# Kernel optimization log

Hardware: AMD Instinct MI355X
Metric: run time of the kernel (lower is better)

The kernel has to match this reference:

```python
import jax, jax.numpy as jnp
import numpy as np

H = 128
N_CAN = 100000
N_FLAG = 50000
E = 600000
L = 500000


def _sage_conv(x_src, x_dst, edge_index, Wl, bl, Wr):
    # PyG SAGEConv (mean aggr): lin_l(mean_{j in N(i)} x_j) + lin_r(x_i)
    src, dst = edge_index[0], edge_index[1]
    msg = x_src[src]                                        # [E, H] gather
    n_dst = x_dst.shape[0]
    agg = jax.ops.segment_sum(msg, dst, num_segments=n_dst)  # [N_dst, H]
    cnt = jax.ops.segment_sum(jnp.ones((msg.shape[0],), msg.dtype), dst,
                              num_segments=n_dst)
    mean = agg / jnp.maximum(cnt, 1.0)[:, None]
    return mean @ Wl.T + bl + x_dst @ Wr.T


def setup_inputs() -> dict:
    key = jax.random.key(0)
    ks = jax.random.split(key, 16)
    s = 1.0 / np.sqrt(H)
    inp = {
        'can_node_id': jnp.arange(N_CAN, dtype=jnp.int64) if jax.config.jax_enable_x64 else jnp.arange(N_CAN, dtype=jnp.int32),
        'flag_node_id': jnp.arange(N_FLAG, dtype=jnp.int32),
        'edge_index_cf': jnp.stack([
            jax.random.randint(ks[0], (E,), 0, N_CAN),
            jax.random.randint(ks[1], (E,), 0, N_FLAG)]),
        'edge_index_fc': jnp.stack([
            jax.random.randint(ks[2], (E,), 0, N_FLAG),
            jax.random.randint(ks[3], (E,), 0, N_CAN)]),
        'edge_label_index': jnp.stack([
            jax.random.randint(ks[4], (L,), 0, N_CAN),
            jax.random.randint(ks[5], (L,), 0, N_FLAG)]),
        'can_emb': jax.random.normal(ks[6], (N_CAN, H), jnp.float32),
        'flag_emb': jax.random.normal(ks[7], (N_FLAG, H), jnp.float32),
        # SAGEConv for edge type CAN->flag (updates flag nodes)
        'Wl_cf': jax.random.normal(ks[8], (H, H), jnp.float32) * s,
        'bl_cf': jnp.zeros((H,), jnp.float32),
        'Wr_cf': jax.random.normal(ks[9], (H, H), jnp.float32) * s,
        # SAGEConv for edge type flag->CAN (updates CAN nodes)
        'Wl_fc': jax.random.normal(ks[10], (H, H), jnp.float32) * s,
        'bl_fc': jnp.zeros((H,), jnp.float32),
        'Wr_fc': jax.random.normal(ks[11], (H, H), jnp.float32) * s,
        # classifier MLP
        'W1': jax.random.normal(ks[12], (H, 2 * H), jnp.float32) * (1.0 / np.sqrt(2 * H)),
        'b1': jnp.zeros((H,), jnp.float32),
        'W2': jax.random.normal(ks[13], (1, H), jnp.float32) * s,
        'b2': jnp.zeros((1,), jnp.float32),
    }
    return inp


def reference(can_node_id, flag_node_id, edge_index_cf, edge_index_fc,
              edge_label_index, can_emb, flag_emb,
              Wl_cf, bl_cf, Wr_cf, Wl_fc, bl_fc, Wr_fc,
              W1, b1, W2, b2):
    # embedding lookups
    x_can = can_emb[can_node_id]    # [N_CAN, H]
    x_flag = flag_emb[flag_node_id]  # [N_FLAG, H]
    # to_hetero single SAGE layer + relu (dropout is identity in eval)
    upd_flag = jax.nn.relu(_sage_conv(x_can, x_flag, edge_index_cf, Wl_cf, bl_cf, Wr_cf))
    upd_can = jax.nn.relu(_sage_conv(x_flag, x_can, edge_index_fc, Wl_fc, bl_fc, Wr_fc))
    # link prediction classifier
    src = upd_can[edge_label_index[0]]   # [L, H]
    dst = upd_flag[edge_label_index[1]]  # [L, H]
    h = jax.nn.relu(jnp.concatenate([src, dst], axis=-1) @ W1.T + b1)
    out = h @ W2.T + b2
    return out.reshape(-1)
```

## Files before the change

### kernel.cpp

```cpp
#include <hip/hip_runtime.h>
#include <hip/hip_bf16.h>

#define H 128
#define BSH 8
#define MAXB 1024
#define PCH 1024
#define PIT (PCH / 256)

typedef __attribute__((ext_vector_type(8))) short short8;
typedef __attribute__((ext_vector_type(4))) short short4v;
typedef __attribute__((ext_vector_type(4))) float floatx4;
typedef unsigned short ushort_t;
typedef unsigned int uint_t;

__device__ __forceinline__ short f2bf(float f) {
    __hip_bfloat16 h = __float2bfloat16(f);
    return *reinterpret_cast<short*>(&h);
}
__device__ __forceinline__ float bflo(uint_t u) { return __uint_as_float(u << 16); }
__device__ __forceinline__ float bfhi(uint_t u) { return __uint_as_float(u & 0xFFFF0000u); }
__device__ __forceinline__ uint_t pack_bf2(float x, float y) {
    return (uint_t)(ushort_t)f2bf(x) | ((uint_t)(ushort_t)f2bf(y) << 16);
}
__device__ __forceinline__ void acc8(float* acc, uint4 r) {
    acc[0] += bflo(r.x); acc[1] += bfhi(r.x);
    acc[2] += bflo(r.y); acc[3] += bfhi(r.y);
    acc[4] += bflo(r.z); acc[5] += bfhi(r.z);
    acc[6] += bflo(r.w); acc[7] += bfhi(r.w);
}

__global__ __launch_bounds__(256)
void bucket_hist_cvt_kernel(const int* __restrict__ ei1, const int* __restrict__ ei2,
                            int E, int NF, int B, int* __restrict__ bcnt, int nbh,
                            const float* __restrict__ a, int n4a,
                            const float* __restrict__ b, int n4b,
                            ushort_t* __restrict__ da, ushort_t* __restrict__ db,
                            const float* __restrict__ Wl_cf, const float* __restrict__ Wr_cf,
                            const float* __restrict__ Wl_fc, const float* __restrict__ Wr_fc,
                            const float* __restrict__ W1, ushort_t* __restrict__ wb) {
    __shared__ int h[MAXB];
    int tid = threadIdx.x;
    if ((int)blockIdx.x < nbh) {
        for (int i = tid; i < B; i += 256) h[i] = 0;
        __syncthreads();
        int base = blockIdx.x * PCH;
        #pragma unroll
        for (int it = 0; it < PIT; ++it) {
            int t = base + it * 256 + tid;
            if (t < 2 * E) {
                int g = (t < E) ? ei1[E + t] : (ei2[E + t - E] + NF);
                atomicAdd(&h[g >> BSH], 1);
            }
        }
        __syncthreads();
        for (int i = tid; i < B; i += 256)
            if (h[i]) atomicAdd(&bcnt[i], h[i]);
        return;
    }
    int i = ((int)blockIdx.x - nbh) * 256 + tid;
    const float* src; ushort_t* dst; int k;
    if (i < n4a) { src = a; dst = da; k = i; }
    else if (i < n4a + n4b) { src = b; dst = db; k = i - n4a; }
    else {
        int idx = (i - n4a - n4b) * 4;
        if (idx >= 98304) return;
        int off;
        if      (idx < 16384) { src = Wl_cf; off = idx; }
        else if (idx < 32768) { src = Wr_cf; off = idx - 16384; }
        else if (idx < 49152) { src = Wl_fc; off = idx - 32768; }
        else if (idx < 65536) { src = Wr_fc; off = idx - 49152; }
        else                  { src = W1;    off = idx - 65536; }
        float4 v = *(const float4*)(src + off);
        short4v s;
        s[0] = f2bf(v.x); s[1] = f2bf(v.y); s[2] = f2bf(v.z); s[3] = f2bf(v.w);
        *(short4v*)(wb + idx) = s;
        return;
    }
    float4 v = ((const float4*)src)[k];
    short4v s;
    s[0] = f2bf(v.x); s[1] = f2bf(v.y); s[2] = f2bf(v.z); s[3] = f2bf(v.w);
    ((short4v*)dst)[k] = s;
}

__global__ __launch_bounds__(256)
void partition_kernel(const int* __restrict__ ei1, const int* __restrict__ ei2,
                      int E, int NF, int B, const int* __restrict__ bcnt,
                      int* __restrict__ bfront, uint_t* __restrict__ part) {
    __shared__ int h[MAXB];
    __shared__ int basex[MAXB];
    __shared__ int sdata[256];
    int tid = threadIdx.x;
    {
        int base4 = tid * 4;
        int v[4]; int s = 0;
        #pragma unroll
        for (int i = 0; i < 4; ++i) { int idx = base4 + i; v[i] = (idx < B) ? bcnt[idx] : 0; s += v[i]; }
        sdata[tid] = s;
        __syncthreads();
        for (int off = 1; off < 256; off <<= 1) {
            int t = (tid >= off) ? sdata[tid - off] : 0;
            __syncthreads();
            sdata[tid] += t;
            __syncthreads();
        }
        int excl = tid ? sdata[tid - 1] : 0;
        #pragma unroll
        for (int i = 0; i < 4; ++i) {
            int idx = base4 + i;
            if (idx < B) basex[idx] = excl;
            excl += v[i];
        }
    }
    for (int i = tid; i < B; i += 256) h[i] = 0;
    __syncthreads();
    int base = blockIdx.x * PCH;
    #pragma unroll
    for (int it = 0; it < PIT; ++it) {
        int t = base + it * 256 + tid;
        if (t < 2 * E) {
            int g = (t < E) ? ei1[E + t] : (ei2[E + t - E] + NF);
            atomicAdd(&h[g >> BSH], 1);
        }
    }
    __syncthreads();
    for (int i = tid; i < B; i += 256) {
        int c = h[i];
        if (c) basex[i] += atomicAdd(&bfront[i], c);
    }
    __syncthreads();
    for (int i = tid; i < B; i += 256) h[i] = 0;
    __syncthreads();
    #pragma unroll
    for (int it = 0; it < PIT; ++it) {
        int t = base + it * 256 + tid;
        if (t < 2 * E) {
            int g, s;
            if (t < E) { g = ei1[E + t]; s = ei1[t]; }
            else       { int e = t - E; g = ei2[E + e] + NF; s = ei2[e]; }
            int bk = g >> BSH;
            int r = atomicAdd(&h[bk], 1);
            part[basex[bk] + r] = ((uint_t)(g & 255) << 24) | (uint_t)s;
        }
    }
}

__global__ __launch_bounds__(256)
void fine_bin_kernel(const int* __restrict__ bcnt, int B, int nTot, int E2,
                     const uint_t* __restrict__ part,
                     int* __restrict__ offs, int* __restrict__ bins) {
    __shared__ int cnt[256];
    __shared__ int sdata[256];
    __shared__ int excl[256];
    int b = blockIdx.x;
    int tid = threadIdx.x;
    {
        int partial = 0;
        for (int i = tid; i < b; i += 256) partial += bcnt[i];
        sdata[tid] = partial;
        __syncthreads();
        for (int off = 128; off > 0; off >>= 1) {
            if (tid < off) sdata[tid] += sdata[tid + off];
            __syncthreads();
        }
    }
    int seg0 = sdata[0];
    int seg1 = seg0 + bcnt[b];
    int gbase = b << BSH;
    __syncthreads();
    cnt[tid] = 0;
    __syncthreads();
    for (int k = seg0 + tid; k < seg1; k += 256)
        atomicAdd(&cnt[part[k] >> 24], 1);
    __syncthreads();
    sdata[tid] = cnt[tid];
    __syncthreads();
    for (int off = 1; off < 256; off <<= 1) {
        int t = (tid >= off) ? sdata[tid - off] : 0;
        __syncthreads();
        sdata[tid] += t;
        __syncthreads();
    }
    excl[tid] = tid ? sdata[tid - 1] : 0;
    int g = gbase + tid;
    if (g < nTot) offs[g] = seg0 + excl[tid];
    if (b == 0 && tid == 0) offs[nTot] = E2;
    cnt[tid] = 0;
    __syncthreads();
    for (int k = seg0 + tid; k < seg1; k += 256) {
        uint_t e = part[k];
        int l = (int)(e >> 24);
        int r = atomicAdd(&cnt[l], 1);
        bins[seg0 + excl[l] + r] = (int)(e & 0x00FFFFFFu);
    }
}

__global__ __launch_bounds__(256)
void gather_mean16_kernel(const int* __restrict__ offs, int nTotal, int split,
                          const int* __restrict__ bins,
                          const ushort_t* __restrict__ embA, ushort_t* __restrict__ aggA,
                          const ushort_t* __restrict__ embB, ushort_t* __restrict__ aggB) {
    int g = blockIdx.x * 16 + (threadIdx.x >> 4);
    if (g >= nTotal) return;
    int l15 = threadIdx.x & 15;
    int start = offs[g];
    int end = offs[g + 1];
    int deg = end - start;
    const ushort_t* emb; ushort_t* agg; int row;
    if (g < split) { emb = embA; agg = aggA; row = g; }
    else           { emb = embB; agg = aggB; row = g - split; }

    float acc[8];
    #pragma unroll
    for (int t = 0; t < 8; ++t) acc[t] = 0.f;

    const ushort_t* ep = emb + l15 * 8;
    int nPre = deg < 16 ? deg : 16;
    int pre = (l15 < nPre) ? bins[start + l15] : 0;

    int k = 0;
    for (; k + 3 < nPre; k += 4) {
        int s0 = __shfl(pre, k,     16);
        int s1 = __shfl(pre, k + 1, 16);
        int s2 = __shfl(pre, k + 2, 16);
        int s3 = __shfl(pre, k + 3, 16);
        uint4 r0 = *(const uint4*)(ep + (size_t)s0 * H);
        uint4 r1 = *(const uint4*)(ep + (size_t)s1 * H);
        uint4 r2 = *(const uint4*)(ep + (size_t)s2 * H);
        uint4 r3 = *(const uint4*)(ep + (size_t)s3 * H);
        acc8(acc, r0); acc8(acc, r1); acc8(acc, r2); acc8(acc, r3);
    }
    for (; k < nPre; ++k) {
        int s = __shfl(pre, k, 16);
        uint4 r = *(const uint4*)(ep + (size_t)s * H);
        acc8(acc, r);
    }
    for (int kk = start + 16; kk < end; ++kk) {
        int s = bins[kk];
        uint4 r = *(const uint4*)(ep + (size_t)s * H);
        acc8(acc, r);
    }

    float inv = 1.0f / fmaxf((float)deg, 1.0f);
    uint4 o;
    o.x = pack_bf2(acc[0] * inv, acc[1] * inv);
    o.y = pack_bf2(acc[2] * inv, acc[3] * inv);
    o.z = pack_bf2(acc[4] * inv, acc[5] * inv);
    o.w = pack_bf2(acc[6] * inv, acc[7] * inv);
    *(uint4*)(agg + (size_t)row * H + l15 * 8) = o;
}

__global__ __launch_bounds__(256)
void sage3_kernel(int nbF, int NF, int NC,
                  ushort_t* __restrict__ aggf, const ushort_t* __restrict__ embf,
                  ushort_t* __restrict__ aggc, const ushort_t* __restrict__ embc,
                  const ushort_t* __restrict__ wlf, const ushort_t* __restrict__ wrf,
                  const float* __restrict__ blf,
                  const ushort_t* __restrict__ wlc, const ushort_t* __restrict__ wrc,
                  const float* __restrict__ blc,
                  const ushort_t* __restrict__ W1) {
    __shared__ short A[64][136];
    bool isF = (int)blockIdx.x < nbF;
    int nrows = isF ? NF : NC;
    int rbase = (isF ? blockIdx.x : blockIdx.x - nbF) * 64;
    ushort_t* io = isF ? aggf : aggc;
    const ushort_t* emb = isF ? embf : embc;
    const ushort_t* Wl = isF ? wlf : wlc;
    const ushort_t* Wr = isF ? wrf : wrc;
    const float* bl = isF ? blf : blc;
    int koff = isF ? 128 : 0;

    int tid = threadIdx.x;
    int lane = tid & 63;
    int wv = tid >> 6;
    int l15 = lane & 15;
    int quad = lane >> 4;
    int nb0 = 32 * wv + l15;

    floatx4 acc[4][2];
    #pragma unroll
    for (int i = 0; i < 4; ++i)
        #pragma unroll
        for (int j = 0; j < 2; ++j)
            acc[i][j] = (floatx4){0.f, 0.f, 0.f, 0.f};

    float blv0 = bl[nb0];
    float blv1 = bl[nb0 + 16];

    for (int idx = tid; idx < 64 * 16; idx += 256) {
        int r = idx >> 4, c = idx & 15;
        int row = rbase + r;
        uint4 v = (uint4){0u, 0u, 0u, 0u};
        if (row < nrows) v = *(const uint4*)(io + (size_t)row * H + c * 8);
        *(uint4*)&A[r][c * 8] = v;
    }
    __syncthreads();
    #pragma unroll
    for (int ks = 0; ks < 4; ++ks) {
        int kb = ks * 32 + quad * 8;
        short8 b0 = *(const short8*)(Wl + (size_t)nb0 * H + kb);
        short8 b1 = *(const short8*)(Wl + (size_t)(nb0 + 16) * H + kb);
        #pragma unroll
        for (int mt = 0; mt < 4; ++mt) {
            short8 a = *(const short8*)&A[16 * mt + l15][kb];
            acc[mt][0] = __builtin_amdgcn_mfma_f32_16x16x32_bf16(a, b0, acc[mt][0], 0, 0, 0);
            acc[mt][1] = __builtin_amdgcn_mfma_f32_16x16x32_bf16(a, b1, acc[mt][1], 0, 0, 0);
        }
    }
    __syncthreads();

    for (int idx = tid; idx < 64 * 16; idx += 256) {
        int r = idx >> 4, c = idx & 15;
        int row = rbase + r;
        uint4 v = (uint4){0u, 0u, 0u, 0u};
        if (row < nrows) v = *(const uint4*)(emb + (size_t)row * H + c * 8);
        *(uint4*)&A[r][c * 8] = v;
    }
    __syncthreads();
    #pragma unroll
    for (int ks = 0; ks < 4; ++ks) {
        int kb = ks * 32 + quad * 8;
        short8 b0 = *(const short8*)(Wr + (size_t)nb0 * H + kb);
        short8 b1 = *(const short8*)(Wr + (size_t)(nb0 + 16) * H + kb);
        #pragma unroll
        for (int mt = 0; mt < 4; ++mt) {
            short8 a = *(const short8*)&A[16 * mt + l15][kb];
            acc[mt][0] = __builtin_amdgcn_mfma_f32_16x16x32_bf16(a, b0, acc[mt][0], 0, 0, 0);
            acc[mt][1] = __builtin_amdgcn_mfma_f32_16x16x32_bf16(a, b1, acc[mt][1], 0, 0, 0);
        }
    }
    __syncthreads();

    #pragma unroll
    for (int mt = 0; mt < 4; ++mt)
        #pragma unroll
        for (int nt = 0; nt < 2; ++nt) {
            float blv = nt ? blv1 : blv0;
            int colw = nb0 + 16 * nt;
            #pragma unroll
            for (int rg = 0; rg < 4; ++rg) {
                int row = 16 * mt + quad * 4 + rg;
                A[row][colw] = f2bf(fmaxf(acc[mt][nt][rg] + blv, 0.0f));
                acc[mt][nt][rg] = 0.0f;
            }
        }
    __syncthreads();

    const ushort_t* W1p = W1 + koff;
    #pragma unroll
    for (int ks = 0; ks < 4; ++ks) {
        int kb = ks * 32 + quad * 8;
        short8 b0 = *(const short8*)(W1p + (size_t)nb0 * 256 + kb);
        short8 b1 = *(const short8*)(W1p + (size_t)(nb0 + 16) * 256 + kb);
        #pragma unroll
        for (int mt = 0; mt < 4; ++mt) {
            short8 a = *(const short8*)&A[16 * mt + l15][kb];
            acc[mt][0] = __builtin_amdgcn_mfma_f32_16x16x32_bf16(a, b0, acc[mt][0], 0, 0, 0);
            acc[mt][1] = __builtin_amdgcn_mfma_f32_16x16x32_bf16(a, b1, acc[mt][1], 0, 0, 0);
        }
    }

    #pragma unroll
    for (int mt = 0; mt < 4; ++mt)
        #pragma unroll
        for (int rg = 0; rg < 4; ++rg) {
            int row = rbase + 16 * mt + quad * 4 + rg;
            if (row < nrows) {
                io[(size_t)row * H + nb0]      = (ushort_t)f2bf(acc[mt][0][rg]);
                io[(size_t)row * H + nb0 + 16] = (ushort_t)f2bf(acc[mt][1][rg]);
            }
        }
}

__global__ __launch_bounds__(256)
void hist2_kernel(const int* __restrict__ ei1, const int* __restrict__ ei2, int E,
                  int* __restrict__ deg1, int* __restrict__ deg2) {
    int t = blockIdx.x * 256 + threadIdx.x;
    if (t < E) atomicAdd(&deg1[ei1[E + t]], 1);
    else if (t < 2 * E) { int e = t - E; atomicAdd(&deg2[ei2[E + e]], 1); }
}

__global__ __launch_bounds__(256)
void scan_blocksum_kernel(const int* __restrict__ deg, int n, int* __restrict__ bsums) {
    __shared__ int sdata[256];
    int tid = threadIdx.x;
    int base = blockIdx.x * 1024 + tid * 4;
    int v = 0;
    #pragma unroll
    for (int i = 0; i < 4; ++i) { int idx = base + i; if (idx < n) v += deg[idx]; }
    sdata[tid] = v;
    __syncthreads();
    for (int off = 128; off > 0; off >>= 1) {
        if (tid < off) sdata[tid] += sdata[tid + off];
        __syncthreads();
    }
    if (tid == 0) bsums[blockIdx.x] = sdata[0];
}

__global__ __launch_bounds__(256)
void scan_write_kernel(int* __restrict__ data, int n, const int* __restrict__ bsums) {
    __shared__ int sdata[256];
    __shared__ int boff;
    int tid = threadIdx.x;
    if (tid < 64) {
        int acc = 0;
        for (int i = tid; i < (int)blockIdx.x; i += 64) acc += bsums[i];
        #pragma unroll
        for (int off = 32; off > 0; off >>= 1) acc += __shfl_xor(acc, off, 64);
        if (tid == 0) boff = acc;
    }
    int base = blockIdx.x * 1024 + tid * 4;
    int v[4]; int s = 0;
    #pragma unroll
    for (int i = 0; i < 4; ++i) { int idx = base + i; v[i] = (idx < n) ? data[idx] : 0; s += v[i]; }
    sdata[tid] = s;
    __syncthreads();
    for (int off = 1; off < 256; off <<= 1) {
        int t = (tid >= off) ? sdata[tid - off] : 0;
        __syncthreads();
        sdata[tid] += t;
        __syncthreads();
    }
    int excl = (tid == 0 ? 0 : sdata[tid - 1]) + boff;
    #pragma unroll
    for (int i = 0; i < 4; ++i) {
        int idx = base + i;
        if (idx < n) data[idx] = excl;
        excl += v[i];
    }
}

__global__ __launch_bounds__(256)
void incl_to_start_kernel(const int* __restrict__ incl, int nTot, int* __restrict__ offs) {
    int g = blockIdx.x * 256 + threadIdx.x;
    if (g < nTot) offs[g + 1] = incl[g];
    if (g == 0) offs[0] = 0;
}

__global__ __launch_bounds__(256)
void bin2_kernel(const int* __restrict__ ei1, const int* __restrict__ ei2, int E,
                 int* __restrict__ offs1, int* __restrict__ offs2,
                 int* __restrict__ bins) {
    int t = blockIdx.x * 256 + threadIdx.x;
    if (t < E) {
        int pos = atomicAdd(&offs1[ei1[E + t]], 1);
        bins[pos] = ei1[t];
    } else if (t < 2 * E) {
        int e = t - E;
        int pos = atomicAdd(&offs2[ei2[E + e]], 1);
        bins[pos] = ei2[e];
    }
}

__global__ __launch_bounds__(256)
void classify_kernel(const int* __restrict__ eli, int L,
                     const ushort_t* __restrict__ u_can,
                     const ushort_t* __restrict__ u_flag,
                     const float* __restrict__ b1,
                     const float* __restrict__ W2,
                     const float* __restrict__ b2,
                     float* __restrict__ out) {
    int tid = threadIdx.x;
    int lane = tid & 63;
    int wv = tid >> 6;
    int sub = lane >> 4;
    int l15 = lane & 15;
    int p = blockIdx.x * 16 + wv * 4 + sub;
    if (p >= L) return;
    int i = eli[p];
    int j = eli[L + p];
    uint4 a = ((const uint4*)(u_can  + (size_t)i * H))[l15];
    uint4 b = ((const uint4*)(u_flag + (size_t)j * H))[l15];
    float4 bb0 = ((const float4*)b1)[l15 * 2];
    float4 bb1 = ((const float4*)b1)[l15 * 2 + 1];
    float4 w0  = ((const float4*)W2)[l15 * 2];
    float4 w1  = ((const float4*)W2)[l15 * 2 + 1];
    float s = fmaxf(bflo(a.x) + bflo(b.x) + bb0.x, 0.f) * w0.x
            + fmaxf(bfhi(a.x) + bfhi(b.x) + bb0.y, 0.f) * w0.y
            + fmaxf(bflo(a.y) + bflo(b.y) + bb0.z, 0.f) * w0.z
            + fmaxf(bfhi(a.y) + bfhi(b.y) + bb0.w, 0.f) * w0.w
            + fmaxf(bflo(a.z) + bflo(b.z) + bb1.x, 0.f) * w1.x
            + fmaxf(bfhi(a.z) + bfhi(b.z) + bb1.y, 0.f) * w1.y
            + fmaxf(bflo(a.w) + bflo(b.w) + bb1.z, 0.f) * w1.z
            + fmaxf(bfhi(a.w) + bfhi(b.w) + bb1.w, 0.f) * w1.w;
    #pragma unroll
    for (int off = 8; off > 0; off >>= 1)
        s += __shfl_down(s, off, 16);
    if (l15 == 0) out[p] = s + b2[0];
}

extern "C" void kernel_launch(void* const* d_in, const int* in_sizes, int n_in,
                              void* d_out, int out_size, void* d_ws, size_t ws_size,
                              hipStream_t stream) {
    const int*   ei_cf    = (const int*)d_in[2];
    const int*   ei_fc    = (const int*)d_in[3];
    const int*   eli      = (const int*)d_in[4];
    const float* can_emb  = (const float*)d_in[5];
    const float* flag_emb = (const float*)d_in[6];
    const float* Wl_cf    = (const float*)d_in[7];
    const float* bl_cf    = (const float*)d_in[8];
    const float* Wr_cf    = (const float*)d_in[9];
    const float* Wl_fc    = (const float*)d_in[10];
    const float* bl_fc    = (const float*)d_in[11];
    const float* Wr_fc    = (const float*)d_in[12];
    const float* W1       = (const float*)d_in[13];
    const float* b1       = (const float*)d_in[14];
    const float* W2       = (const float*)d_in[15];
    const float* b2       = (const float*)d_in[16];
    float* out = (float*)d_out;

    const int NCAN  = in_sizes[0];
    const int NFLAG = in_sizes[1];
    const int E     = in_sizes[2] / 2;
    const int L     = in_sizes[4] / 2;
    const int nTot  = NCAN + NFLAG;
    const int B     = (nTot + 255) >> BSH;

    ushort_t* aggc = (ushort_t*)d_ws;
    ushort_t* aggf = aggc + (size_t)NCAN * H;
    ushort_t* embc = aggf + (size_t)NFLAG * H;
    ushort_t* embf = embc + (size_t)NCAN * H;
    char* tail = (char*)(embf + (size_t)NFLAG * H);
    size_t tail_off = (size_t)(tail - (char*)d_ws);

    int nbF = (NFLAG + 63) / 64, nbC = (NCAN + 63) / 64;
    int n4c = NCAN * H / 4, n4f = NFLAG * H / 4;
    int nbcvt = (n4c + n4f + 24576 + 255) / 256;

    size_t off_offs  = tail_off;
    size_t off_bcnt  = off_offs  + (size_t)(nTot + 1) * 4;
    size_t off_bfrnt = off_bcnt  + (size_t)MAXB * 4;
    size_t off_bins  = off_bfrnt + (size_t)MAXB * 4;
    size_t off_part  = off_bins  + (size_t)2 * E * 4;
    size_t off_wb    = off_part  + (size_t)2 * E * 4;
    size_t need_new  = off_wb + 98304 * 2;

    int* offs   = (int*)((char*)d_ws + off_offs);
    int* bcnt   = (int*)((char*)d_ws + off_bcnt);
    int* bfront = (int*)((char*)d_ws + off_bfrnt);
    int* bins   = (int*)((char*)d_ws + off_bins);

    if (ws_size >= need_new && B <= MAXB) {
        uint_t* part = (uint_t*)((char*)d_ws + off_part);
        ushort_t* wb = (ushort_t*)((char*)d_ws + off_wb);
        ushort_t* wb_wlcf = wb, *wb_wrcf = wb + 16384, *wb_wlfc = wb + 32768,
                 *wb_wrfc = wb + 49152, *wb_w1 = wb + 65536;

        int nbh = (2 * E + PCH - 1) / PCH;
        hipMemsetAsync(bcnt, 0, (size_t)2 * MAXB * 4, stream);
        bucket_hist_cvt_kernel<<<nbh + nbcvt, 256, 0, stream>>>(
            ei_cf, ei_fc, E, NFLAG, B, bcnt, nbh,
            can_emb, n4c, flag_emb, n4f, embc, embf,
            Wl_cf, Wr_cf, Wl_fc, Wr_fc, W1, wb);
        partition_kernel<<<nbh, 256, 0, stream>>>(ei_cf, ei_fc, E, NFLAG, B, bcnt, bfront, part);
        fine_bin_kernel<<<B, 256, 0, stream>>>(bcnt, B, nTot, 2 * E, part, offs, bins);
        gather_mean16_kernel<<<(nTot + 15) / 16, 256, 0, stream>>>(
            offs, nTot, NFLAG, bins, embc, aggf, embf, aggc);
        sage3_kernel<<<nbF + nbC, 256, 0, stream>>>(
            nbF, NFLAG, NCAN, aggf, embf, aggc, embc,
            wb_wlcf, wb_wrcf, bl_cf, wb_wlfc, wb_wrfc, bl_fc, wb_w1);
    } else {
        int* scanf_ = bins;
        int* scanc_ = scanf_ + NFLAG;
        int* bins2  = scanc_ + NCAN;
        int* bsums  = bins2 + 2 * E;
        ushort_t* wb = (ushort_t*)(bsums + 256);
        ushort_t* wb_wlcf = wb, *wb_wrcf = wb + 16384, *wb_wlfc = wb + 32768,
                 *wb_wrfc = wb + 49152, *wb_w1 = wb + 65536;

        bucket_hist_cvt_kernel<<<nbcvt, 256, 0, stream>>>(
            ei_cf, ei_fc, E, NFLAG, B, bcnt, 0,
            can_emb, n4c, flag_emb, n4f, embc, embf,
            Wl_cf, Wr_cf, Wl_fc, Wr_fc, W1, wb);
        hipMemsetAsync(scanf_, 0, ((size_t)NFLAG + NCAN) * 4, stream);
        int nb = (nTot + 1023) / 1024;
        hist2_kernel<<<(2 * E + 255) / 256, 256, 0, stream>>>(ei_cf, ei_fc, E, scanf_, scanc_);
        scan_blocksum_kernel<<<nb, 256, 0, stream>>>(scanf_, nTot, bsums);
        scan_write_kernel<<<nb, 256, 0, stream>>>(scanf_, nTot, bsums);
        bin2_kernel<<<(2 * E + 255) / 256, 256, 0, stream>>>(ei_cf, ei_fc, E, scanf_, scanc_, bins2);
        incl_to_start_kernel<<<(nTot + 255) / 256, 256, 0, stream>>>(scanf_, nTot, offs);
        gather_mean16_kernel<<<(nTot + 15) / 16, 256, 0, stream>>>(
            offs, nTot, NFLAG, bins2, embc, aggf, embf, aggc);
        sage3_kernel<<<nbF + nbC, 256, 0, stream>>>(
            nbF, NFLAG, NCAN, aggf, embf, aggc, embc,
            wb_wlcf, wb_wrcf, bl_cf, wb_wlfc, wb_wrfc, bl_fc, wb_w1);
    }

    classify_kernel<<<(L + 15) / 16, 256, 0, stream>>>(
        eli, L, aggc, aggf, b1, W2, b2, out);
}
```

Before: 346.4 us.

## Replace two-level bucket partition with global atomic histogram, scan and binning

This removes the bucketed partition pipeline: the coarse histogram, the partition into buckets, and the per-bucket fine binning. Edges are now binned to CSR with a direct global-atomic degree histogram, a two-kernel scan and an atomic scatter pass. The scan now runs in place on offs+1, so the extra incl-to-start kernel goes away, and the embedding and weight conversion becomes its own kernel. The aim is fewer passes and simpler kernels, at the cost of scattered global atomics and scattered writes with worse locality.

```diff
diff --git a/kernel.cpp b/kernel.cpp
--- a/kernel.cpp
+++ b/kernel.cpp
@@ -2,10 +2,6 @@
 #include <hip/hip_bf16.h>
 
 #define H 128
-#define BSH 8
-#define MAXB 1024
-#define PCH 1024
-#define PIT (PCH / 256)
 
 typedef __attribute__((ext_vector_type(8))) short short8;
 typedef __attribute__((ext_vector_type(4))) short short4v;
@@ -30,34 +26,13 @@
 }
 
 __global__ __launch_bounds__(256)
-void bucket_hist_cvt_kernel(const int* __restrict__ ei1, const int* __restrict__ ei2,
-                            int E, int NF, int B, int* __restrict__ bcnt, int nbh,
-                            const float* __restrict__ a, int n4a,
-                            const float* __restrict__ b, int n4b,
-                            ushort_t* __restrict__ da, ushort_t* __restrict__ db,
-                            const float* __restrict__ Wl_cf, const float* __restrict__ Wr_cf,
-                            const float* __restrict__ Wl_fc, const float* __restrict__ Wr_fc,
-                            const float* __restrict__ W1, ushort_t* __restrict__ wb) {
-    __shared__ int h[MAXB];
-    int tid = threadIdx.x;
-    if ((int)blockIdx.x < nbh) {
-        for (int i = tid; i < B; i += 256) h[i] = 0;
-        __syncthreads();
-        int base = blockIdx.x * PCH;
-        #pragma unroll
-        for (int it = 0; it < PIT; ++it) {
-            int t = base + it * 256 + tid;
-            if (t < 2 * E) {
-                int g = (t < E) ? ei1[E + t] : (ei2[E + t - E] + NF);
-                atomicAdd(&h[g >> BSH], 1);
-            }
-        }
-        __syncthreads();
-        for (int i = tid; i < B; i += 256)
-            if (h[i]) atomicAdd(&bcnt[i], h[i]);
-        return;
-    }
-    int i = ((int)blockIdx.x - nbh) * 256 + tid;
+void cvt_kernel(const float* __restrict__ a, int n4a,
+                const float* __restrict__ b, int n4b,
+                ushort_t* __restrict__ da, ushort_t* __restrict__ db,
+                const float* __restrict__ Wl_cf, const float* __restrict__ Wr_cf,
+                const float* __restrict__ Wl_fc, const float* __restrict__ Wr_fc,
+                const float* __restrict__ W1, ushort_t* __restrict__ wb) {
+    int i = (int)blockIdx.x * 256 + threadIdx.x;
     const float* src; ushort_t* dst; int k;
     if (i < n4a) { src = a; dst = da; k = i; }
     else if (i < n4a + n4b) { src = b; dst = db; k = i - n4a; }
@@ -83,96 +58,47 @@
 }
 
 __global__ __launch_bounds__(256)
-void partition_kernel(const int* __restrict__ ei1, const int* __restrict__ ei2,
-                      int E, int NF, int B, const int* __restrict__ bcnt,
-                      int* __restrict__ bfront, uint_t* __restrict__ part) {
-    __shared__ int h[MAXB];
-    __shared__ int basex[MAXB];
+void hist2_kernel(const int* __restrict__ ei1, const int* __restrict__ ei2, int E,
+                  int* __restrict__ deg1, int* __restrict__ deg2) {
+    int t = blockIdx.x * 256 + threadIdx.x;
+    if (t < E) atomicAdd(&deg1[ei1[E + t]], 1);
+    else if (t < 2 * E) { int e = t - E; atomicAdd(&deg2[ei2[E + e]], 1); }
+}
+
+__global__ __launch_bounds__(256)
+void scan_blocksum_kernel(const int* __restrict__ deg, int n, int* __restrict__ bsums) {
     __shared__ int sdata[256];
     int tid = threadIdx.x;
-    {
-        int base4 = tid * 4;
-        int v[4]; int s = 0;
-        #pragma unroll
-        for (int i = 0; i < 4; ++i) { int idx = base4 + i; v[i] = (idx < B) ? bcnt[idx] : 0; s += v[i]; }
-        sdata[tid] = s;
+    int base = blockIdx.x * 1024 + tid * 4;
+    int v = 0;
+    #pragma unroll
+    for (int i = 0; i < 4; ++i) { int idx = base + i; if (idx < n) v += deg[idx]; }
+    sdata[tid] = v;
+    __syncthreads();
+    for (int off = 128; off > 0; off >>= 1) {
+        if (tid < off) sdata[tid] += sdata[tid + off];
         __syncthreads();
-        for (int off = 1; off < 256; off <<= 1) {
-            int t = (tid >= off) ? sdata[tid - off] : 0;
-            __syncthreads();
-            sdata[tid] += t;
-            __syncthreads();
-        }
-        int excl = tid ? sdata[tid - 1] : 0;
-        #pragma unroll
-        for (int i = 0; i < 4; ++i) {
-            int idx = base4 + i;
-            if (idx < B) basex[idx] = excl;
-            excl += v[i];
-        }
-    }
-    for (int i = tid; i < B; i += 256) h[i] = 0;
-    __syncthreads();
-    int base = blockIdx.x * PCH;
-    #pragma unroll
-    for (int it = 0; it < PIT; ++it) {
-        int t = base + it * 256 + tid;
-        if (t < 2 * E) {
-            int g = (t < E) ? ei1[E + t] : (ei2[E + t - E] + NF);
-            atomicAdd(&h[g >> BSH], 1);
-        }
-    }
-    __syncthreads();
-    for (int i = tid; i < B; i += 256) {
-        int c = h[i];
-        if (c) basex[i] += atomicAdd(&bfront[i], c);
-    }
-    __syncthreads();
-    for (int i = tid; i < B; i += 256) h[i] = 0;
-    __syncthreads();
-    #pragma unroll
-    for (int it = 0; it < PIT; ++it) {
-        int t = base + it * 256 + tid;
-        if (t < 2 * E) {
-            int g, s;
-            if (t < E) { g = ei1[E + t]; s = ei1[t]; }
-            else       { int e = t - E; g = ei2[E + e] + NF; s = ei2[e]; }
-            int bk = g >> BSH;
-            int r = atomicAdd(&h[bk], 1);
-            part[basex[bk] + r] = ((uint_t)(g & 255) << 24) | (uint_t)s;
-        }
-    }
-}
-
-__global__ __launch_bounds__(256)
-void fine_bin_kernel(const int* __restrict__ bcnt, int B, int nTot, int E2,
-                     const uint_t* __restrict__ part,
-                     int* __restrict__ offs, int* __restrict__ bins) {
-    __shared__ int cnt[256];
+    }
+    if (tid == 0) bsums[blockIdx.x] = sdata[0];
+}
+
+__global__ __launch_bounds__(256)
+void scan_write_kernel(int* __restrict__ data, int n, const int* __restrict__ bsums) {
     __shared__ int sdata[256];
-    __shared__ int excl[256];
-    int b = blockIdx.x;
+    __shared__ int boff;
     int tid = threadIdx.x;
-    {
-        int partial = 0;
-        for (int i = tid; i < b; i += 256) partial += bcnt[i];
-        sdata[tid] = partial;
-        __syncthreads();
-        for (int off = 128; off > 0; off >>= 1) {
-            if (tid < off) sdata[tid] += sdata[tid + off];
-            __syncthreads();
-        }
-    }
-    int seg0 = sdata[0];
-    int seg1 = seg0 + bcnt[b];
-    int gbase = b << BSH;
-    __syncthreads();
-    cnt[tid] = 0;
-    __syncthreads();
-    for (int k = seg0 + tid; k < seg1; k += 256)
-        atomicAdd(&cnt[part[k] >> 24], 1);
-    __syncthreads();
-    sdata[tid] = cnt[tid];
+    if (tid < 64) {
+        int acc = 0;
+        for (int i = tid; i < (int)blockIdx.x; i += 64) acc += bsums[i];
+        #pragma unroll
+        for (int off = 32; off > 0; off >>= 1) acc += __shfl_xor(acc, off, 64);
+        if (tid == 0) boff = acc;
+    }
+    int base = blockIdx.x * 1024 + tid * 4;
+    int v[4]; int s = 0;
+    #pragma unroll
+    for (int i = 0; i < 4; ++i) { int idx = base + i; v[i] = (idx < n) ? data[idx] : 0; s += v[i]; }
+    sdata[tid] = s;
     __syncthreads();
     for (int off = 1; off < 256; off <<= 1) {
         int t = (tid >= off) ? sdata[tid - off] : 0;
@@ -180,17 +106,27 @@
         sdata[tid] += t;
         __syncthreads();
     }
-    excl[tid] = tid ? sdata[tid - 1] : 0;
-    int g = gbase + tid;
-    if (g < nTot) offs[g] = seg0 + excl[tid];
-    if (b == 0 && tid == 0) offs[nTot] = E2;
-    cnt[tid] = 0;
-    __syncthreads();
-    for (int k = seg0 + tid; k < seg1; k += 256) {
-        uint_t e = part[k];
-        int l = (int)(e >> 24);
-        int r = atomicAdd(&cnt[l], 1);
-        bins[seg0 + excl[l] + r] = (int)(e & 0x00FFFFFFu);
+    int excl = (tid == 0 ? 0 : sdata[tid - 1]) + boff;
+    #pragma unroll
+    for (int i = 0; i < 4; ++i) {
+        int idx = base + i;
+        if (idx < n) data[idx] = excl;
+        excl += v[i];
+    }
+}
+
+__global__ __launch_bounds__(256)
+void bin2_kernel(const int* __restrict__ ei1, const int* __restrict__ ei2, int E,
+                 int* __restrict__ offs1, int* __restrict__ offs2,
+                 int* __restrict__ bins) {
+    int t = blockIdx.x * 256 + threadIdx.x;
+    if (t < E) {
+        int pos = atomicAdd(&offs1[ei1[E + t]], 1);
+        bins[pos] = ei1[t];
+    } else if (t < 2 * E) {
+        int e = t - E;
+        int pos = atomicAdd(&offs2[ei2[E + e]], 1);
+        bins[pos] = ei2[e];
     }
 }
 
@@ -369,86 +305,6 @@
                 io[(size_t)row * H + nb0 + 16] = (ushort_t)f2bf(acc[mt][1][rg]);
             }
         }
-}
-
-__global__ __launch_bounds__(256)
-void hist2_kernel(const int* __restrict__ ei1, const int* __restrict__ ei2, int E,
-                  int* __restrict__ deg1, int* __restrict__ deg2) {
-    int t = blockIdx.x * 256 + threadIdx.x;
-    if (t < E) atomicAdd(&deg1[ei1[E + t]], 1);
-    else if (t < 2 * E) { int e = t - E; atomicAdd(&deg2[ei2[E + e]], 1); }
-}
-
-__global__ __launch_bounds__(256)
-void scan_blocksum_kernel(const int* __restrict__ deg, int n, int* __restrict__ bsums) {
-    __shared__ int sdata[256];
-    int tid = threadIdx.x;
-    int base = blockIdx.x * 1024 + tid * 4;
-    int v = 0;
-    #pragma unroll
-    for (int i = 0; i < 4; ++i) { int idx = base + i; if (idx < n) v += deg[idx]; }
-    sdata[tid] = v;
-    __syncthreads();
-    for (int off = 128; off > 0; off >>= 1) {
-        if (tid < off) sdata[tid] += sdata[tid + off];
-        __syncthreads();
-    }
-    if (tid == 0) bsums[blockIdx.x] = sdata[0];
-}
-
-__global__ __launch_bounds__(256)
-void scan_write_kernel(int* __restrict__ data, int n, const int* __restrict__ bsums) {
-    __shared__ int sdata[256];
-    __shared__ int boff;
-    int tid = threadIdx.x;
-    if (tid < 64) {
-        int acc = 0;
-        for (int i = tid; i < (int)blockIdx.x; i += 64) acc += bsums[i];
-        #pragma unroll
-        for (int off = 32; off > 0; off >>= 1) acc += __shfl_xor(acc, off, 64);
-        if (tid == 0) boff = acc;
-    }
-    int base = blockIdx.x * 1024 + tid * 4;
-    int v[4]; int s = 0;
-    #pragma unroll
-    for (int i = 0; i < 4; ++i) { int idx = base + i; v[i] = (idx < n) ? data[idx] : 0; s += v[i]; }
-    sdata[tid] = s;
-    __syncthreads();
-    for (int off = 1; off < 256; off <<= 1) {
-        int t = (tid >= off) ? sdata[tid - off] : 0;
-        __syncthreads();
-        sdata[tid] += t;
-        __syncthreads();
-    }
-    int excl = (tid == 0 ? 0 : sdata[tid - 1]) + boff;
-    #pragma unroll
-    for (int i = 0; i < 4; ++i) {
-        int idx = base + i;
-        if (idx < n) data[idx] = excl;
-        excl += v[i];
-    }
-}
-
-__global__ __launch_bounds__(256)
-void incl_to_start_kernel(const int* __restrict__ incl, int nTot, int* __restrict__ offs) {
-    int g = blockIdx.x * 256 + threadIdx.x;
-    if (g < nTot) offs[g + 1] = incl[g];
-    if (g == 0) offs[0] = 0;
-}
-
-__global__ __launch_bounds__(256)
-void bin2_kernel(const int* __restrict__ ei1, const int* __restrict__ ei2, int E,
-                 int* __restrict__ offs1, int* __restrict__ offs2,
-                 int* __restrict__ bins) {
-    int t = blockIdx.x * 256 + threadIdx.x;
-    if (t < E) {
-        int pos = atomicAdd(&offs1[ei1[E + t]], 1);
-        bins[pos] = ei1[t];
-    } else if (t < 2 * E) {
-        int e = t - E;
-        int pos = atomicAdd(&offs2[ei2[E + e]], 1);
-        bins[pos] = ei2[e];
-    }
 }
 
 __global__ __launch_bounds__(256)
@@ -513,78 +369,39 @@
     const int E     = in_sizes[2] / 2;
     const int L     = in_sizes[4] / 2;
     const int nTot  = NCAN + NFLAG;
-    const int B     = (nTot + 255) >> BSH;
 
     ushort_t* aggc = (ushort_t*)d_ws;
     ushort_t* aggf = aggc + (size_t)NCAN * H;
     ushort_t* embc = aggf + (size_t)NFLAG * H;
     ushort_t* embf = embc + (size_t)NCAN * H;
-    char* tail = (char*)(embf + (size_t)NFLAG * H);
-    size_t tail_off = (size_t)(tail - (char*)d_ws);
+
+    int* offs = (int*)(embf + (size_t)NFLAG * H);
+    int* bins = offs + (nTot + 1);
+    ushort_t* wb = (ushort_t*)(bins + (size_t)2 * E);
+    ushort_t* wb_wlcf = wb, *wb_wrcf = wb + 16384, *wb_wlfc = wb + 32768,
+             *wb_wrfc = wb + 49152, *wb_w1 = wb + 65536;
+    int* bsums = bins;
 
     int nbF = (NFLAG + 63) / 64, nbC = (NCAN + 63) / 64;
     int n4c = NCAN * H / 4, n4f = NFLAG * H / 4;
     int nbcvt = (n4c + n4f + 24576 + 255) / 256;
-
-    size_t off_offs  = tail_off;
-    size_t off_bcnt  = off_offs  + (size_t)(nTot + 1) * 4;
-    size_t off_bfrnt = off_bcnt  + (size_t)MAXB * 4;
-    size_t off_bins  = off_bfrnt + (size_t)MAXB * 4;
-    size_t off_part  = off_bins  + (size_t)2 * E * 4;
-    size_t off_wb    = off_part  + (size_t)2 * E * 4;
-    size_t need_new  = off_wb + 98304 * 2;
-
-    int* offs   = (int*)((char*)d_ws + off_offs);
-    int* bcnt   = (int*)((char*)d_ws + off_bcnt);
-    int* bfront = (int*)((char*)d_ws + off_bfrnt);
-    int* bins   = (int*)((char*)d_ws + off_bins);
-
-    if (ws_size >= need_new && B <= MAXB) {
-        uint_t* part = (uint_t*)((char*)d_ws + off_part);
-        ushort_t* wb = (ushort_t*)((char*)d_ws + off_wb);
-        ushort_t* wb_wlcf = wb, *wb_wrcf = wb + 16384, *wb_wlfc = wb + 32768,
-                 *wb_wrfc = wb + 49152, *wb_w1 = wb + 65536;
-
-        int nbh = (2 * E + PCH - 1) / PCH;
-        hipMemsetAsync(bcnt, 0, (size_t)2 * MAXB * 4, stream);
-        bucket_hist_cvt_kernel<<<nbh + nbcvt, 256, 0, stream>>>(
-            ei_cf, ei_fc, E, NFLAG, B, bcnt, nbh,
-            can_emb, n4c, flag_emb, n4f, embc, embf,
-            Wl_cf, Wr_cf, Wl_fc, Wr_fc, W1, wb);
-        partition_kernel<<<nbh, 256, 0, stream>>>(ei_cf, ei_fc, E, NFLAG, B, bcnt, bfront, part);
-        fine_bin_kernel<<<B, 256, 0, stream>>>(bcnt, B, nTot, 2 * E, part, offs, bins);
-        gather_mean16_kernel<<<(nTot + 15) / 16, 256, 0, stream>>>(
-            offs, nTot, NFLAG, bins, embc, aggf, embf, aggc);
-        sage3_kernel<<<nbF + nbC, 256, 0, stream>>>(
-            nbF, NFLAG, NCAN, aggf, embf, aggc, embc,
-            wb_wlcf, wb_wrcf, bl_cf, wb_wlfc, wb_wrfc, bl_fc, wb_w1);
-    } else {
-        int* scanf_ = bins;
-        int* scanc_ = scanf_ + NFLAG;
-        int* bins2  = scanc_ + NCAN;
-        int* bsums  = bins2 + 2 * E;
-        ushort_t* wb = (ushort_t*)(bsums + 256);
-        ushort_t* wb_wlcf = wb, *wb_wrcf = wb + 16384, *wb_wlfc = wb + 32768,
-                 *wb_wrfc = wb + 49152, *wb_w1 = wb + 65536;
-
-        bucket_hist_cvt_kernel<<<nbcvt, 256, 0, stream>>>(
-            ei_cf, ei_fc, E, NFLAG, B, bcnt, 0,
-            can_emb, n4c, flag_emb, n4f, embc, embf,
-            Wl_cf, Wr_cf, Wl_fc, Wr_fc, W1, wb);
-        hipMemsetAsync(scanf_, 0, ((size_t)NFLAG + NCAN) * 4, stream);
-        int nb = (nTot + 1023) / 1024;
-        hist2_kernel<<<(2 * E + 255) / 256, 256, 0, stream>>>(ei_cf, ei_fc, E, scanf_, scanc_);
-        scan_blocksum_kernel<<<nb, 256, 0, stream>>>(scanf_, nTot, bsums);
-        scan_write_kernel<<<nb, 256, 0, stream>>>(scanf_, nTot, bsums);
-        bin2_kernel<<<(2 * E + 255) / 256, 256, 0, stream>>>(ei_cf, ei_fc, E, scanf_, scanc_, bins2);
-        incl_to_start_kernel<<<(nTot + 255) / 256, 256, 0, stream>>>(scanf_, nTot, offs);
-        gather_mean16_kernel<<<(nTot + 15) / 16, 256, 0, stream>>>(
-            offs, nTot, NFLAG, bins2, embc, aggf, embf, aggc);
-        sage3_kernel<<<nbF + nbC, 256, 0, stream>>>(
-            nbF, NFLAG, NCAN, aggf, embf, aggc, embc,
-            wb_wlcf, wb_wrcf, bl_cf, wb_wlfc, wb_wrfc, bl_fc, wb_w1);
-    }
-
+    int nbE = (2 * E + 255) / 256;
+    int nbScan = (nTot + 1023) / 1024;
+
+    hipMemsetAsync(offs, 0, (size_t)(nTot + 1) * 4, stream);
+
+    cvt_kernel<<<nbcvt, 256, 0, stream>>>(
+        can_emb, n4c, flag_emb, n4f, embc, embf,
+        Wl_cf, Wr_cf, Wl_fc, Wr_fc, W1, wb);
+    hist2_kernel<<<nbE, 256, 0, stream>>>(ei_cf, ei_fc, E, offs + 1, offs + 1 + NFLAG);
+    scan_blocksum_kernel<<<nbScan, 256, 0, stream>>>(offs + 1, nTot, bsums);
+    scan_write_kernel<<<nbScan, 256, 0, stream>>>(offs + 1, nTot, bsums);
+    bin2_kernel<<<nbE, 256, 0, stream>>>(ei_cf, ei_fc, E, offs + 1, offs + 1 + NFLAG, bins);
+    gather_mean16_kernel<<<(nTot + 15) / 16, 256, 0, stream>>>(
+        offs, nTot, NFLAG, bins, embc, aggf, embf, aggc);
+    sage3_kernel<<<nbF + nbC, 256, 0, stream>>>(
+        nbF, NFLAG, NCAN, aggf, embf, aggc, embc,
+        wb_wlcf, wb_wrcf, bl_cf, wb_wlfc, wb_wrfc, bl_fc, wb_w1);
     classify_kernel<<<(L + 15) / 16, 256, 0, stream>>>(
         eli, L, aggc, aggf, b1, W2, b2, out);
 }
```

New measurement: 415.9 us. 1.2x slower.
